# Optimization experiments

Hardware: AMD Instinct MI355X
Metric: run time of the kernel (lower is better)

Reference implementation:

```python
import jax, jax.numpy as jnp
import numpy as np

B, S, D = 2, 2048, 1024
H, DK, DV = 16, 64, 64
DFF = 4096
EPS_RMS = 1e-6


def setup_inputs() -> dict:
    key = jax.random.key(0)
    ks = jax.random.split(key, 10)
    sc = 0.02
    return {
        "x": jax.random.normal(ks[0], (B, S, D), jnp.float32),
        "w_q": jax.random.normal(ks[1], (D, H * DK), jnp.float32) * sc,
        "w_k": jax.random.normal(ks[2], (D, H * DK), jnp.float32) * sc,
        "w_v": jax.random.normal(ks[3], (D, H * DV), jnp.float32) * sc,
        "w_o": jax.random.normal(ks[4], (H * DV, D), jnp.float32) * sc,
        "w_gate": jax.random.normal(ks[5], (D, DFF), jnp.float32) * sc,
        "w_up": jax.random.normal(ks[6], (D, DFF), jnp.float32) * sc,
        "w_down": jax.random.normal(ks[7], (DFF, D), jnp.float32) * sc,
        "g1": jnp.ones((D,), jnp.float32),
        "g2": jnp.ones((D,), jnp.float32),
    }


def _rmsnorm(x, g):
    var = jnp.mean(jnp.square(x), axis=-1, keepdims=True)
    return x * jax.lax.rsqrt(var + EPS_RMS) * g


def _stable_softmax(s):
    # Faithful to source: exp(x) / (sum exp(x) + 1e-9); fully-masked rows -> 0.
    e = jnp.exp(s)
    return e / (jnp.sum(e, axis=-1, keepdims=True) + 1e-9)


def reference(x, w_q, w_k, w_v, w_o, w_gate, w_up, w_down, g1, g2):
    b, s, d = x.shape
    h = _rmsnorm(x, g1)
    q = (h @ w_q).reshape(b, s, H, DK).transpose(0, 2, 1, 3)  # [B,H,S,DK]
    k = (h @ w_k).reshape(b, s, H, DK).transpose(0, 2, 1, 3)
    v = (h @ w_v).reshape(b, s, H, DV).transpose(0, 2, 1, 3)
    scores = jnp.einsum("bhqd,bhkd->bhqk", q, k) / jnp.sqrt(jnp.asarray(DK, x.dtype))
    # triu with diagonal=0: self and future positions are masked
    mask = jnp.triu(jnp.ones((s, s), bool))
    scores = jnp.where(mask, -jnp.inf, scores)
    attn = _stable_softmax(scores)  # [B,H,S,S]
    av = jnp.einsum("bhqk,bhkd->bhqd", attn, v)
    av = av.transpose(0, 2, 1, 3).reshape(b, s, H * DV)
    x = x + av @ w_o  # residual 1
    h2 = _rmsnorm(x, g2)
    hidden = jax.nn.silu(h2 @ w_gate) * (h2 @ w_up)
    return x + hidden @ w_down  # residual 2
```

## Files before the change

### kernel.cpp

```cpp
#include <hip/hip_runtime.h>
#include <cstdint>
#include <cstddef>

typedef unsigned short u16;
typedef unsigned char u8;
typedef unsigned int u32;
typedef __bf16 bf16x8 __attribute__((ext_vector_type(8)));
typedef float floatx4 __attribute__((ext_vector_type(4)));
typedef float floatx16 __attribute__((ext_vector_type(16)));
typedef int i32x8 __attribute__((ext_vector_type(8)));

#define B_ 2
#define S_ 2048
#define D_ 1024
#define H_ 16
#define DFF_ 4096
#define BS_ 4096

__device__ __forceinline__ u16 f2bf(float f) {
  u32 u = __builtin_bit_cast(u32, f);
  u += 0x7fffu + ((u >> 16) & 1u);
  return (u16)(u >> 16);
}
__device__ __forceinline__ float bf2f(u16 h) {
  u32 u = ((u32)h) << 16;
  return __builtin_bit_cast(float, u);
}

__device__ __forceinline__ u32 cvtpk_bf16(float lo, float hi) {
  u32 r;
  asm("v_cvt_pk_bf16_f32 %0, %1, %2" : "=v"(r) : "v"(lo), "v"(hi));
  return r;
}

__device__ __forceinline__ float fexp2(float x) {
  float r;
  asm("v_exp_f32 %0, %1" : "=v"(r) : "v"(x));
  return r;
}

__device__ __forceinline__ u32 f2e4m3(float f) {
  u32 u = __builtin_bit_cast(u32, f);
  const u32 s = (u >> 24) & 0x80u;
  const u32 au = u & 0x7fffffffu;
  if (au < 0x3c800000u) return s;
  if (au > 0x43e00000u) return s | 0x7eu;
  const u32 lsb = (au >> 20) & 1u;
  const u32 r = au + 0x0007ffffu + lsb;
  const u32 e = (r >> 23) & 0xffu;
  const u32 m = (r >> 20) & 7u;
  return s | (((e - 120u) & 0xfu) << 3) | m;
}

__device__ __forceinline__ void gl_lds16(const void* g, void* l) {
  __builtin_amdgcn_global_load_lds(
      (const __attribute__((address_space(1))) void*)g,
      (__attribute__((address_space(3))) void*)l, 16, 0, 0);
}

__device__ __forceinline__ void xcd_swz(int GX, int GY, int& bx, int& by) {
  int flat = by * GX + bx;
  const int q = (GX * GY) >> 3;
  flat = (flat & 7) * q + (flat >> 3);
  bx = flat % GX;
  by = flat / GX;
}

#define WAITB(N) asm volatile("s_waitcnt vmcnt(" #N ")\n\ts_barrier" ::: "memory")

__global__ void prep_weights(const float* __restrict__ wq, const float* __restrict__ wk,
                             const float* __restrict__ wv, const float* __restrict__ wo,
                             const float* __restrict__ wg, const float* __restrict__ wu,
                             const float* __restrict__ wd,
                             u16* __restrict__ wqkv_t, u16* __restrict__ wo_t,
                             u8* __restrict__ wguf8, u16* __restrict__ wdn_t) {
  __shared__ float tile[32][33];
  const int id = blockIdx.x;
  const float* src;
  u16* dst = nullptr;
  int R, C, bx, by, mode;
  if (id < 3072) {
    const int which = id >> 10, lo = id & 1023;
    src = which == 0 ? wq : (which == 1 ? wk : wv);
    dst = wqkv_t + which * 1024 * 1024;
    R = 1024; C = 1024; bx = lo & 31; by = lo >> 5; mode = 0;
  } else if (id < 4096) {
    const int lo = id - 3072;
    src = wo; dst = wo_t; R = 1024; C = 1024; bx = lo & 31; by = lo >> 5; mode = 0;
  } else if (id < 8192) {
    const int lo = id - 4096;
    src = wg; R = 1024; C = 4096; bx = lo & 127; by = lo >> 7; mode = 1;
  } else if (id < 12288) {
    const int lo = id - 8192;
    src = wu; R = 1024; C = 4096; bx = lo & 127; by = lo >> 7; mode = 2;
  } else {
    const int lo = id - 12288;
    src = wd; dst = wdn_t; R = 4096; C = 1024; bx = lo & 31; by = lo >> 5; mode = 0;
  }
  const int tx = threadIdx.x, ty = threadIdx.y;
  const int c0 = bx * 32, r0 = by * 32;
#pragma unroll
  for (int i = 0; i < 4; i++)
    tile[ty + i * 8][tx] = src[(size_t)(r0 + ty + i * 8) * C + c0 + tx];
  __syncthreads();
  const int sx = ty * 32 + tx;
  const int oci = sx >> 3, cg = (sx & 7) * 4;
  const int oc = c0 + oci;
  const float v0 = tile[cg][oci], v1 = tile[cg + 1][oci];
  const float v2 = tile[cg + 2][oci], v3 = tile[cg + 3][oci];
  if (mode == 0) {
    uint2 o;
    o.x = (u32)f2bf(v0) | ((u32)f2bf(v1) << 16);
    o.y = (u32)f2bf(v2) | ((u32)f2bf(v3) << 16);
    *(uint2*)(dst + (size_t)oc * R + r0 + cg) = o;
  } else {
    const int orow = (oc >> 5) * 64 + (oc & 31) + (mode == 2 ? 32 : 0);
    const u32 p = f2e4m3(v0 * 64.f) | (f2e4m3(v1 * 64.f) << 8) |
                  (f2e4m3(v2 * 64.f) << 16) | (f2e4m3(v3 * 64.f) << 24);
    *(u32*)(wguf8 + (size_t)orow * 1024 + r0 + cg) = p;
  }
}

template <int F8>
__global__ __launch_bounds__(256) void rmsnorm_kernel(const float* __restrict__ x,
                                                      const float* __restrict__ g,
                                                      void* __restrict__ out) {
  const int row = blockIdx.x, t = threadIdx.x;
  const float4 v = ((const float4*)(x + (size_t)row * 1024))[t];
  float ss = v.x * v.x + v.y * v.y + v.z * v.z + v.w * v.w;
#pragma unroll
  for (int off = 32; off > 0; off >>= 1) ss += __shfl_xor(ss, off);
  __shared__ float red[4];
  if ((t & 63) == 0) red[t >> 6] = ss;
  __syncthreads();
  ss = red[0] + red[1] + red[2] + red[3];
  const float inv = rsqrtf(ss * (1.0f / 1024.0f) + 1e-6f);
  const float4 gv = ((const float4*)g)[t];
  const float y0 = v.x * inv * gv.x, y1 = v.y * inv * gv.y;
  const float y2 = v.z * inv * gv.z, y3 = v.w * inv * gv.w;
  if (F8) {
    const u32 p = f2e4m3(y0) | (f2e4m3(y1) << 8) | (f2e4m3(y2) << 16) | (f2e4m3(y3) << 24);
    const int k = t * 4;
    const u32 ofs = (u32)(((row >> 5) * 16 + (k >> 6)) * 2048 +
                          ((k >> 5) & 1) * 1024 + (row & 31) * 32 + (k & 31));
    *(u32*)((u8*)out + ofs) = p;
  } else {
    uint2 o;
    o.x = (u32)f2bf(y0) | ((u32)f2bf(y1) << 16);
    o.y = (u32)f2bf(y2) | ((u32)f2bf(y3) << 16);
    ((uint2*)out)[(size_t)row * 256 + t] = o;
  }
}

template <int BN>
__device__ __forceinline__ void bt_step(const u16* Asb, const u16* Bsb,
                                        floatx16 (&acc)[2][BN / 64],
                                        int wm, int wn, int c31, int khalf) {
  constexpr int NTI = BN / 64;
#pragma unroll
  for (int ks = 0; ks < 4; ks++) {
    bf16x8 af[2], bfr[NTI];
#pragma unroll
    for (int mi = 0; mi < 2; mi++) {
      const int row = wm * 64 + mi * 32 + c31;
      const int e = (ks * 2 + khalf) ^ (row & 7);
      af[mi] = *(const bf16x8*)(Asb + row * 64 + e * 8);
    }
#pragma unroll
    for (int ni = 0; ni < NTI; ni++) {
      const int row = wn * (BN / 2) + ni * 32 + c31;
      const int e = (ks * 2 + khalf) ^ (row & 7);
      bfr[ni] = *(const bf16x8*)(Bsb + row * 64 + e * 8);
    }
#pragma unroll
    for (int mi = 0; mi < 2; mi++)
#pragma unroll
      for (int ni = 0; ni < NTI; ni++)
        acc[mi][ni] = __builtin_amdgcn_mfma_f32_32x32x16_bf16(af[mi], bfr[ni],
                                                              acc[mi][ni], 0, 0, 0);
  }
}

template <int SPW>
__device__ __forceinline__ void bt_issue(const u16* (&gsrc)[SPW], u16* const (&ld0)[SPW],
                                         int bufofs) {
#pragma unroll
  for (int i = 0; i < SPW; i++) gl_lds16(gsrc[i], ld0[i] + bufofs);
#pragma unroll
  for (int i = 0; i < SPW; i++) gsrc[i] += 64;
}

template <int BN, int EPI>
__global__ __launch_bounds__(256) void gemm_bt(const u16* __restrict__ A,
                                               const u16* __restrict__ Bt,
                                               void* __restrict__ Cout,
                                               const float* __restrict__ res,
                                               u16* __restrict__ vTout,
                                               int M, int N, int K) {
  constexpr int NTI = BN / 64;
  constexpr int ASZ = 128 * 64;
  constexpr int STRIDE = ASZ + BN * 64;
  constexpr int NBUF = (BN == 64) ? 3 : 2;
  __shared__ u16 SMEM[NBUF * STRIDE];
  constexpr int NSEG = 16 + BN / 8;
  constexpr int SPW = NSEG / 4;
  const int t = threadIdx.x, w = t >> 6, l = t & 63;

  int bx = (int)blockIdx.x, by = (int)blockIdx.y;
  xcd_swz((int)gridDim.x, (int)gridDim.y, bx, by);
  const int m0 = by * 128, n0 = bx * BN;
  const int wm = w >> 1, wn = w & 1;
  const int c31 = l & 31, khalf = l >> 5;

  const u16* gsrc[SPW];
  u16* ld0[SPW];
  {
    const int rl = l >> 3, ch = (l & 7) ^ rl;
#pragma unroll
    for (int i = 0; i < SPW; i++) {
      const int s = w * SPW + i;
      if (s < 16) {
        gsrc[i] = A + (size_t)(m0 + s * 8 + rl) * K + ch * 8;
        ld0[i] = SMEM + s * 512;
      } else {
        gsrc[i] = Bt + (size_t)(n0 + (s - 16) * 8 + rl) * K + ch * 8;
        ld0[i] = SMEM + ASZ + (s - 16) * 512;
      }
    }
  }

  floatx16 acc[2][NTI] = {};

#define BT_STEP(CB) bt_step<BN>(SMEM + (CB)*STRIDE, SMEM + (CB)*STRIDE + ASZ, \
                                acc, wm, wn, c31, khalf)

  if constexpr (BN == 64) {
    bt_issue<SPW>(gsrc, ld0, 0 * STRIDE);
    bt_issue<SPW>(gsrc, ld0, 1 * STRIDE);
    const int NT = K >> 6;
    for (int rep = 0; rep < (NT - 4) / 3; rep++) {
      WAITB(6); bt_issue<SPW>(gsrc, ld0, 2 * STRIDE); BT_STEP(0);
      WAITB(6); bt_issue<SPW>(gsrc, ld0, 0 * STRIDE); BT_STEP(1);
      WAITB(6); bt_issue<SPW>(gsrc, ld0, 1 * STRIDE); BT_STEP(2);
    }
    WAITB(6); bt_issue<SPW>(gsrc, ld0, 2 * STRIDE); BT_STEP(0);
    WAITB(6); bt_issue<SPW>(gsrc, ld0, 0 * STRIDE); BT_STEP(1);
    WAITB(6); BT_STEP(2);
    WAITB(0); BT_STEP(0);
  } else {
    bt_issue<SPW>(gsrc, ld0, 0 * STRIDE);
    bt_issue<SPW>(gsrc, ld0, 1 * STRIDE);
    const int NT = K >> 6;
    for (int kk = 0; kk < NT - 2; kk += 2) {
      WAITB(8); BT_STEP(0);
      __builtin_amdgcn_s_barrier();
      bt_issue<SPW>(gsrc, ld0, 0 * STRIDE);
      WAITB(8); BT_STEP(1);
      __builtin_amdgcn_s_barrier();
      bt_issue<SPW>(gsrc, ld0, 1 * STRIDE);
    }
    WAITB(8); BT_STEP(0);
    WAITB(0); BT_STEP(1);
  }
#undef BT_STEP

  if constexpr (EPI == 3) {
    if (n0 >= 2048) {
#pragma unroll
      for (int mi = 0; mi < 2; mi++)
#pragma unroll
        for (int ni = 0; ni < NTI; ni++) {
          const int col = n0 + wn * (BN / 2) + ni * 32 + c31 - 2048;
          const int hh = col >> 6, dv = col & 63;
          const int rbase = m0 + wm * 64 + mi * 32 + 4 * khalf;
          const int bb = rbase >> 11;
          u16* vp = vTout + (size_t)((bb * 16 + hh) * 64 + dv) * 2048 + (rbase & 2047);
#pragma unroll
          for (int rg = 0; rg < 4; rg++) {
            uint2 pk;
            pk.x = (u32)f2bf(acc[mi][ni][rg * 4 + 0]) |
                   ((u32)f2bf(acc[mi][ni][rg * 4 + 1]) << 16);
            pk.y = (u32)f2bf(acc[mi][ni][rg * 4 + 2]) |
                   ((u32)f2bf(acc[mi][ni][rg * 4 + 3]) << 16);
            *(uint2*)(vp + rg * 8) = pk;
          }
        }
      return;
    }
  }
#pragma unroll
  for (int mi = 0; mi < 2; mi++)
#pragma unroll
    for (int ni = 0; ni < NTI; ni++) {
      const int col = n0 + wn * (BN / 2) + ni * 32 + c31;
#pragma unroll
      for (int reg = 0; reg < 16; reg++) {
        const int row = m0 + wm * 64 + mi * 32 + (reg & 3) + 8 * (reg >> 2) + 4 * khalf;
        const size_t idx = (size_t)row * N + col;
        if (EPI == 1) ((float*)Cout)[idx] = acc[mi][ni][reg] + res[idx];
        else          ((u16*)Cout)[idx] = f2bf(acc[mi][ni][reg]);
      }
    }
}

__global__ __launch_bounds__(256) void gemm_f8(const u8* __restrict__ Af,
                                               const u8* __restrict__ Bg,
                                               u16* __restrict__ hid,
                                               int M, int K) {
  constexpr int BSZ = 8192;
  __shared__ u8 SMEM[3 * BSZ];
  const int t = threadIdx.x, w = t >> 6, l = t & 63;
  int bx, by;
  {
    const int flat = (int)blockIdx.y * 64 + (int)blockIdx.x;
    const int xcd = flat & 7, seq = flat >> 3;
    const int bxl = seq & 15, byl = (seq >> 4) & 3, bxg = seq >> 6;
    bx = bxg * 16 + bxl;
    by = xcd * 4 + byl;
  }
  const int m0 = by * 128, n0 = bx * 128;
  const int wm = w >> 1, wn = w & 1;
  const int c31 = l & 31, hf = l >> 5;

  const u8* gsrcB[2];
  u32 ldofsB[2];
  {
    const int rl = l >> 2, ch = (l & 3) ^ ((l >> 3) & 3);
#pragma unroll
    for (int i = 0; i < 2; i++) {
      const int s = w * 2 + i;
      gsrcB[i] = Bg + (size_t)(n0 + s * 16 + rl) * K + ch * 16;
      ldofsB[i] = (u32)(s * 1024);
    }
  }
  const u8* Acur[2];
#pragma unroll
  for (int mi = 0; mi < 2; mi++)
    Acur[mi] = Af + (size_t)((by * 4 + wm * 2 + mi) * 16) * 2048 + l * 32;

  floatx16 acc[2][2] = {};
  i32x8 afr[3][2];

#define F8_LDA(SL)                                                      \
  do {                                                                  \
    _Pragma("unroll") for (int mi = 0; mi < 2; mi++) {                  \
      const uint4 lo = *(const uint4*)(Acur[mi]);                       \
      const uint4 hi = *(const uint4*)(Acur[mi] + 16);                  \
      afr[SL][mi] = i32x8{(int)lo.x, (int)lo.y, (int)lo.z, (int)lo.w,   \
                          (int)hi.x, (int)hi.y, (int)hi.z, (int)hi.w};  \
      Acur[mi] += 2048;                                                 \
    }                                                                   \
  } while (0)

#define F8_STB(SL)                                              \
  do {                                                          \
    _Pragma("unroll") for (int i = 0; i < 2; i++) {             \
      gl_lds16(gsrcB[i], SMEM + (SL)*BSZ + ldofsB[i]);          \
      gsrcB[i] += 64;                                           \
    }                                                           \
  } while (0)

#define F8_CMP(SL)                                                             \
  do {                                                                         \
    const u8* Bs = SMEM + (SL)*BSZ;                                            \
    i32x8 bfv[2];                                                              \
    _Pragma("unroll") for (int ni = 0; ni < 2; ni++) {                         \
      const int r = wn * 64 + ni * 32 + c31;                                   \
      const int g = (r >> 1) & 3;                                              \
      const uint4 lo = *(const uint4*)(Bs + r * 64 + ((2 * hf) ^ g) * 16);     \
      const uint4 hi = *(const uint4*)(Bs + r * 64 + ((2 * hf + 1) ^ g) * 16); \
      bfv[ni] = i32x8{(int)lo.x, (int)lo.y, (int)lo.z, (int)lo.w,              \
                      (int)hi.x, (int)hi.y, (int)hi.z, (int)hi.w};             \
    }                                                                          \
    _Pragma("unroll") for (int mi = 0; mi < 2; mi++)                           \
      _Pragma("unroll") for (int ni = 0; ni < 2; ni++)                         \
        acc[mi][ni] = __builtin_amdgcn_mfma_scale_f32_32x32x64_f8f6f4(         \
            afr[SL][mi], bfv[ni], acc[mi][ni], 0, 0,                           \
            0, 0x7F7F7F7F,                                    \
            0, 0x79797979);         \
  } while (0)

  F8_LDA(0); F8_STB(0);
  F8_LDA(1); F8_STB(1);
  for (int rep = 0; rep < 4; rep++) {
    WAITB(6); F8_LDA(2); F8_STB(2); F8_CMP(0);
    WAITB(6); F8_LDA(0); F8_STB(0); F8_CMP(1);
    WAITB(6); F8_LDA(1); F8_STB(1); F8_CMP(2);
  }
  WAITB(6); F8_LDA(2); F8_STB(2); F8_CMP(0);
  WAITB(6); F8_LDA(0); F8_STB(0); F8_CMP(1);
  WAITB(6); F8_CMP(2);
  WAITB(0); F8_CMP(0);
#undef F8_LDA
#undef F8_STB
#undef F8_CMP

#pragma unroll
  for (int mi = 0; mi < 2; mi++) {
    const int colo = (bx * 2 + wn) * 32 + c31;
#pragma unroll
    for (int reg = 0; reg < 16; reg++) {
      const int row = m0 + wm * 64 + mi * 32 + (reg & 3) + 8 * (reg >> 2) + 4 * hf;
      const float g = acc[mi][0][reg];
      const float u = acc[mi][1][reg];
      hid[(size_t)row * 4096 + colo] = f2bf(g / (1.f + __expf(-g)) * u);
    }
  }
}

__global__ __launch_bounds__(256) void attn_kernel(const u16* __restrict__ qkv,
                                                   const u16* __restrict__ vT,
                                                   u16* __restrict__ av) {
  __shared__ u16 SM[2 * 8192];
  __shared__ u16 Ps[4 * 2048];
  const int t = threadIdx.x, w = t >> 6, l = t & 63;
  const int lrow = l & 15, lk = l >> 4;
  const int bh = blockIdx.x;
  const int b = bh >> 4, h = bh & 15;
  u16* Pw = Ps + w * 2048;
  const float SC = 0.125f * 1.44269504088896f;

  for (int pass = 0; pass < 2; pass++) {
    const int qt = pass == 0 ? (15 - (int)blockIdx.y) : (int)blockIdx.y;
    const int qbase = qt * 128 + w * 32;
    const int ktmax = 2 * qt + 1;

    __syncthreads();

    bf16x8 aq[2][2];
#pragma unroll
    for (int sub = 0; sub < 2; sub++)
#pragma unroll
      for (int half = 0; half < 2; half++)
        aq[sub][half] = *(const bf16x8*)(qkv + (size_t)(b * S_ + qbase + sub * 16 + lrow) * 3072 +
                                         h * 64 + half * 32 + lk * 8);

    const u16* gcur[4];
    int gstep[4], loff[4];
#pragma unroll
    for (int i = 0; i < 4; i++) {
      const int c = w + 4 * i;
      const int half = (c >> 2) & 1, grp = c & 3;
      if (c < 8) {
        gcur[i] = qkv + (size_t)(b * S_ + grp * 16 + (l >> 2)) * 3072 + D_ + h * 64 +
                  half * 32 + (l & 3) * 8;
        gstep[i] = 64 * 3072;
        loff[i] = half * 2048 + grp * 512;
      } else {
        gcur[i] = vT + (size_t)(bh * 64 + grp * 16 + (l >> 2)) * S_ + half * 32 + (l & 3) * 8;
        gstep[i] = 64;
        loff[i] = 4096 + half * 2048 + grp * 512;
      }
    }

    floatx4 oacc[2][4] = {};
    float den[2] = {0.f, 0.f};

    int cur = 0;
#pragma unroll
    for (int i = 0; i < 4; i++) { gl_lds16(gcur[i], SM + loff[i]); gcur[i] += gstep[i]; }

    for (int kt = 0; kt <= ktmax; kt++) {
      __syncthreads();
      if (kt < ktmax) {
#pragma unroll
        for (int i = 0; i < 4; i++) {
          gl_lds16(gcur[i], SM + (cur ^ 1) * 8192 + loff[i]);
          gcur[i] += gstep[i];
        }
      }
      const u16* Kbuf = SM + cur * 8192;
      const u16* Vbuf = Kbuf + 4096;

      const bool active = (kt * 64 < qbase + 31);
      if (active) {
        const bool need_mask = (kt * 64 + 64 > qbase);

        bf16x8 bk[4][2];
#pragma unroll
        for (int ct = 0; ct < 4; ct++)
#pragma unroll
          for (int half = 0; half < 2; half++)
            bk[ct][half] = *(const bf16x8*)(Kbuf + half * 2048 + (ct * 16 + lrow) * 32 + lk * 8);

        floatx4 sf[2][4] = {};
        __builtin_amdgcn_s_setprio(1);
#pragma unroll
        for (int sub = 0; sub < 2; sub++)
#pragma unroll
          for (int ct = 0; ct < 4; ct++) {
            sf[sub][ct] = __builtin_amdgcn_mfma_f32_16x16x32_bf16(bk[ct][0], aq[sub][0],
                                                                  sf[sub][ct], 0, 0, 0);
            sf[sub][ct] = __builtin_amdgcn_mfma_f32_16x16x32_bf16(bk[ct][1], aq[sub][1],
                                                                  sf[sub][ct], 0, 0, 0);
          }
        __builtin_amdgcn_s_setprio(0);

        if (!need_mask) {
#pragma unroll
          for (int sub = 0; sub < 2; sub++) {
            const int prow = sub * 16 + lrow;
#pragma unroll
            for (int ct = 0; ct < 4; ct++) {
              const float p0 = fexp2(sf[sub][ct][0] * SC);
              const float p1 = fexp2(sf[sub][ct][1] * SC);
              const float p2 = fexp2(sf[sub][ct][2] * SC);
              const float p3 = fexp2(sf[sub][ct][3] * SC);
              den[sub] += (p0 + p1) + (p2 + p3);
              uint2 pk;
              pk.x = cvtpk_bf16(p0, p1);
              pk.y = cvtpk_bf16(p2, p3);
              *(uint2*)(Pw + prow * 64 + (((2 * ct + (lk >> 1)) ^ (lrow & 7)) << 3) +
                        (lk & 1) * 4) = pk;
            }
          }
        } else {
#pragma unroll
          for (int sub = 0; sub < 2; sub++) {
            const int qp = qbase + sub * 16 + lrow;
            const int prow = sub * 16 + lrow;
#pragma unroll
            for (int ct = 0; ct < 4; ct++) {
              const int kb = kt * 64 + ct * 16 + lk * 4;
              const float p0 = (kb + 0 < qp) ? fexp2(sf[sub][ct][0] * SC) : 0.f;
              const float p1 = (kb + 1 < qp) ? fexp2(sf[sub][ct][1] * SC) : 0.f;
              const float p2 = (kb + 2 < qp) ? fexp2(sf[sub][ct][2] * SC) : 0.f;
              const float p3 = (kb + 3 < qp) ? fexp2(sf[sub][ct][3] * SC) : 0.f;
              den[sub] += (p0 + p1) + (p2 + p3);
              uint2 pk;
              pk.x = cvtpk_bf16(p0, p1);
              pk.y = cvtpk_bf16(p2, p3);
              *(uint2*)(Pw + prow * 64 + (((2 * ct + (lk >> 1)) ^ (lrow & 7)) << 3) +
                        (lk & 1) * 4) = pk;
            }
          }
        }

        bf16x8 ap[2][2], bv[4][2];
#pragma unroll
        for (int sub = 0; sub < 2; sub++)
#pragma unroll
          for (int kh = 0; kh < 2; kh++) {
            const int prow = sub * 16 + lrow;
            ap[sub][kh] = *(const bf16x8*)(Pw + prow * 64 + (((kh * 4 + lk) ^ (prow & 7)) << 3));
          }
#pragma unroll
        for (int ni = 0; ni < 4; ni++)
#pragma unroll
          for (int kh = 0; kh < 2; kh++)
            bv[ni][kh] = *(const bf16x8*)(Vbuf + kh * 2048 + (ni * 16 + lrow) * 32 + lk * 8);
        __builtin_amdgcn_s_setprio(1);
#pragma unroll
        for (int sub = 0; sub < 2; sub++)
#pragma unroll
          for (int ni = 0; ni < 4; ni++) {
            oacc[sub][ni] = __builtin_amdgcn_mfma_f32_16x16x32_bf16(ap[sub][0], bv[ni][0],
                                                                    oacc[sub][ni], 0, 0, 0);
            oacc[sub][ni] = __builtin_amdgcn_mfma_f32_16x16x32_bf16(ap[sub][1], bv[ni][1],
                                                                    oacc[sub][ni], 0, 0, 0);
          }
        __builtin_amdgcn_s_setprio(0);
      }
      cur ^= 1;
    }

#pragma unroll
    for (int sub = 0; sub < 2; sub++) {
      den[sub] += __shfl_xor(den[sub], 16);
      den[sub] += __shfl_xor(den[sub], 32);
    }
    float dq[2][4];
#pragma unroll
    for (int sub = 0; sub < 2; sub++)
#pragma unroll
      for (int r = 0; r < 4; r++)
        dq[sub][r] = __shfl(den[sub], lk * 4 + r);

#pragma unroll
    for (int sub = 0; sub < 2; sub++)
#pragma unroll
      for (int ni = 0; ni < 4; ni++)
#pragma unroll
        for (int r = 0; r < 4; r++) {
          const int row = qbase + sub * 16 + lk * 4 + r;
          const int col = h * 64 + ni * 16 + lrow;
          av[(size_t)(b * S_ + row) * 1024 + col] = f2bf(oacc[sub][ni][r] / (dq[sub][r] + 1e-9f));
        }
  }
}

#define OFF_WQKV 0u
#define OFF_WO   6291456u
#define OFF_WGU8 8388608u
#define OFF_WDN  16777216u
#define OFF_H1   25165824u
#define OFF_QKV  33554432u
#define OFF_VT   58720256u
#define OFF_AV   67108864u
#define OFF_X1   75497472u
#define OFF_H2F8 92274688u
#define OFF_HID  96468992u

extern "C" void kernel_launch(void* const* d_in, const int* in_sizes, int n_in,
                              void* d_out, int out_size, void* d_ws, size_t ws_size,
                              hipStream_t stream) {
  const float* x      = (const float*)d_in[0];
  const float* w_q    = (const float*)d_in[1];
  const float* w_k    = (const float*)d_in[2];
  const float* w_v    = (const float*)d_in[3];
  const float* w_o    = (const float*)d_in[4];
  const float* w_gate = (const float*)d_in[5];
  const float* w_up   = (const float*)d_in[6];
  const float* w_down = (const float*)d_in[7];
  const float* g1     = (const float*)d_in[8];
  const float* g2     = (const float*)d_in[9];

  char* ws = (char*)d_ws;
  u16* wqkv_t = (u16*)(ws + OFF_WQKV);
  u16* wo_t   = (u16*)(ws + OFF_WO);
  u8*  wguf8  = (u8*)(ws + OFF_WGU8);
  u16* wdn_t  = (u16*)(ws + OFF_WDN);
  u16* h1     = (u16*)(ws + OFF_H1);
  u16* qkv    = (u16*)(ws + OFF_QKV);
  u16* vT     = (u16*)(ws + OFF_VT);
  u16* av     = (u16*)(ws + OFF_AV);
  float* x1   = (float*)(ws + OFF_X1);
  u8*  h2f8   = (u8*)(ws + OFF_H2F8);
  u16* hid    = (u16*)(ws + OFF_HID);
  float* out  = (float*)d_out;

  prep_weights<<<16384, dim3(32, 8), 0, stream>>>(w_q, w_k, w_v, w_o, w_gate, w_up, w_down,
                                                  wqkv_t, wo_t, wguf8, wdn_t);

  rmsnorm_kernel<0><<<BS_, 256, 0, stream>>>(x, g1, h1);
  gemm_bt<128, 3><<<dim3(3072 / 128, BS_ / 128), 256, 0, stream>>>(
      h1, wqkv_t, qkv, nullptr, vT, BS_, 3072, 1024);
  attn_kernel<<<dim3(32, 8), 256, 0, stream>>>(qkv, vT, av);
  gemm_bt<64, 1><<<dim3(1024 / 64, BS_ / 128), 256, 0, stream>>>(
      av, wo_t, x1, x, nullptr, BS_, 1024, 1024);
  rmsnorm_kernel<1><<<BS_, 256, 0, stream>>>(x1, g2, h2f8);
  gemm_f8<<<dim3(64, 32), 256, 0, stream>>>(h2f8, wguf8, hid, BS_, 1024);
  gemm_bt<64, 1><<<dim3(1024 / 64, BS_ / 128), 256, 0, stream>>>(
      hid, wdn_t, out, x1, nullptr, BS_, 1024, 4096);
}
```

Baseline: 337.3 us.

## Restructure attention to single-wave blocks loading K/V directly from global

Attention blocks change from 4-wave blocks, which share K/V tiles through double-buffered LDS with barriers and process two paired query tiles, to single-wave blocks each owning 32 query rows. K and V are now read straight from global memory into registers, with K prefetched one tile ahead using ping-pong register sets. This removes block-level synchronisation and gives 2048 small blocks for finer load balance under the causal mask. In exchange, cross-wave reuse of K/V in LDS is lost, so global/L2 traffic rises, and the explicit balanced pairing of short and long query tiles is gone.

```diff
diff --git a/kernel.cpp b/kernel.cpp
--- a/kernel.cpp
+++ b/kernel.cpp
@@ -408,185 +408,148 @@
   }
 }
 
-__global__ __launch_bounds__(256) void attn_kernel(const u16* __restrict__ qkv,
-                                                   const u16* __restrict__ vT,
-                                                   u16* __restrict__ av) {
-  __shared__ u16 SM[2 * 8192];
-  __shared__ u16 Ps[4 * 2048];
-  const int t = threadIdx.x, w = t >> 6, l = t & 63;
+__device__ __forceinline__ void attn_ldK(bf16x8 (&dst)[4][2], const u16* kbase, int kt) {
+#pragma unroll
+  for (int ct = 0; ct < 4; ct++)
+#pragma unroll
+    for (int hf = 0; hf < 2; hf++)
+      dst[ct][hf] = *(const bf16x8*)(kbase + (size_t)(kt * 64 + ct * 16) * 3072 + hf * 32);
+}
+__device__ __forceinline__ void attn_ldV(bf16x8 (&dst)[4][2], const u16* vbase, int kt) {
+#pragma unroll
+  for (int ni = 0; ni < 4; ni++)
+#pragma unroll
+    for (int kh = 0; kh < 2; kh++)
+      dst[ni][kh] = *(const bf16x8*)(vbase + (size_t)(ni * 16) * 2048 + kt * 64 + kh * 32);
+}
+
+__global__ __launch_bounds__(64, 2) void attn_kernel(const u16* __restrict__ qkv,
+                                                     const u16* __restrict__ vT,
+                                                     u16* __restrict__ av) {
+  __shared__ u16 Pw[2048];
+  const int l = threadIdx.x;
   const int lrow = l & 15, lk = l >> 4;
   const int bh = blockIdx.x;
+  const int j = blockIdx.y;
   const int b = bh >> 4, h = bh & 15;
-  u16* Pw = Ps + w * 2048;
+  const int qbase = j * 32;
+  const int NT = (qbase + 30) / 64 + 1;
   const float SC = 0.125f * 1.44269504088896f;
 
-  for (int pass = 0; pass < 2; pass++) {
-    const int qt = pass == 0 ? (15 - (int)blockIdx.y) : (int)blockIdx.y;
-    const int qbase = qt * 128 + w * 32;
-    const int ktmax = 2 * qt + 1;
-
-    __syncthreads();
-
-    bf16x8 aq[2][2];
-#pragma unroll
-    for (int sub = 0; sub < 2; sub++)
-#pragma unroll
-      for (int half = 0; half < 2; half++)
-        aq[sub][half] = *(const bf16x8*)(qkv + (size_t)(b * S_ + qbase + sub * 16 + lrow) * 3072 +
-                                         h * 64 + half * 32 + lk * 8);
-
-    const u16* gcur[4];
-    int gstep[4], loff[4];
-#pragma unroll
-    for (int i = 0; i < 4; i++) {
-      const int c = w + 4 * i;
-      const int half = (c >> 2) & 1, grp = c & 3;
-      if (c < 8) {
-        gcur[i] = qkv + (size_t)(b * S_ + grp * 16 + (l >> 2)) * 3072 + D_ + h * 64 +
-                  half * 32 + (l & 3) * 8;
-        gstep[i] = 64 * 3072;
-        loff[i] = half * 2048 + grp * 512;
-      } else {
-        gcur[i] = vT + (size_t)(bh * 64 + grp * 16 + (l >> 2)) * S_ + half * 32 + (l & 3) * 8;
-        gstep[i] = 64;
-        loff[i] = 4096 + half * 2048 + grp * 512;
+  bf16x8 aq[2][2];
+#pragma unroll
+  for (int sub = 0; sub < 2; sub++)
+#pragma unroll
+    for (int half = 0; half < 2; half++)
+      aq[sub][half] = *(const bf16x8*)(qkv + (size_t)(b * S_ + qbase + sub * 16 + lrow) * 3072 +
+                                       h * 64 + half * 32 + lk * 8);
+
+  const u16* kbase = qkv + (size_t)(b * S_ + lrow) * 3072 + D_ + h * 64 + lk * 8;
+  const u16* vbase = vT + (size_t)(bh * 64 + lrow) * 2048 + lk * 8;
+
+  floatx4 oacc[2][4] = {};
+  float den[2] = {0.f, 0.f};
+
+#define ATTN_BODY(KC, KN, KT, DOLOADN)                                         \
+  do {                                                                         \
+    bf16x8 bv[4][2];                                                           \
+    attn_ldV(bv, vbase, (KT));                                                 \
+    if (DOLOADN) attn_ldK(KN, kbase, (KT) + 1);                                \
+    floatx4 sf[2][4] = {};                                                     \
+    __builtin_amdgcn_s_setprio(1);                                             \
+    _Pragma("unroll") for (int sub = 0; sub < 2; sub++)                        \
+      _Pragma("unroll") for (int ct = 0; ct < 4; ct++) {                       \
+        sf[sub][ct] = __builtin_amdgcn_mfma_f32_16x16x32_bf16(                 \
+            KC[ct][0], aq[sub][0], sf[sub][ct], 0, 0, 0);                      \
+        sf[sub][ct] = __builtin_amdgcn_mfma_f32_16x16x32_bf16(                 \
+            KC[ct][1], aq[sub][1], sf[sub][ct], 0, 0, 0);                      \
+      }                                                                        \
+    __builtin_amdgcn_s_setprio(0);                                             \
+    if ((KT)*64 + 64 <= qbase) {                                               \
+      _Pragma("unroll") for (int sub = 0; sub < 2; sub++) {                    \
+        const int prow = sub * 16 + lrow;                                      \
+        _Pragma("unroll") for (int ct = 0; ct < 4; ct++) {                     \
+          const float p0 = fexp2(sf[sub][ct][0] * SC);                         \
+          const float p1 = fexp2(sf[sub][ct][1] * SC);                         \
+          const float p2 = fexp2(sf[sub][ct][2] * SC);                         \
+          const float p3 = fexp2(sf[sub][ct][3] * SC);                         \
+          den[sub] += (p0 + p1) + (p2 + p3);                                   \
+          uint2 pk;                                                            \
+          pk.x = cvtpk_bf16(p0, p1);                                           \
+          pk.y = cvtpk_bf16(p2, p3);                                           \
+          *(uint2*)(Pw + prow * 64 + (((2 * ct + (lk >> 1)) ^ (lrow & 7)) << 3) + \
+                    (lk & 1) * 4) = pk;                                        \
+        }                                                                      \
+      }                                                                        \
+    } else {                                                                   \
+      _Pragma("unroll") for (int sub = 0; sub < 2; sub++) {                    \
+        const int qp = qbase + sub * 16 + lrow;                                \
+        const int prow = sub * 16 + lrow;                                      \
+        _Pragma("unroll") for (int ct = 0; ct < 4; ct++) {                     \
+          const int kb = (KT) * 64 + ct * 16 + lk * 4;                         \
+          const float p0 = (kb + 0 < qp) ? fexp2(sf[sub][ct][0] * SC) : 0.f;   \
+          const float p1 = (kb + 1 < qp) ? fexp2(sf[sub][ct][1] * SC) : 0.f;   \
+          const float p2 = (kb + 2 < qp) ? fexp2(sf[sub][ct][2] * SC) : 0.f;   \
+          const float p3 = (kb + 3 < qp) ? fexp2(sf[sub][ct][3] * SC) : 0.f;   \
+          den[sub] += (p0 + p1) + (p2 + p3);                                   \
+          uint2 pk;                                                            \
+          pk.x = cvtpk_bf16(p0, p1);                                           \
+          pk.y = cvtpk_bf16(p2, p3);                                           \
+          *(uint2*)(Pw + prow * 64 + (((2 * ct + (lk >> 1)) ^ (lrow & 7)) << 3) + \
+                    (lk & 1) * 4) = pk;                                        \
+        }                                                                      \
+      }                                                                        \
+    }                                                                          \
+    bf16x8 ap[2][2];                                                           \
+    _Pragma("unroll") for (int sub = 0; sub < 2; sub++)                        \
+      _Pragma("unroll") for (int kh = 0; kh < 2; kh++) {                       \
+        const int prow = sub * 16 + lrow;                                      \
+        ap[sub][kh] = *(const bf16x8*)(Pw + prow * 64 +                        \
+                                       (((kh * 4 + lk) ^ (prow & 7)) << 3));   \
+      }                                                                        \
+    __builtin_amdgcn_s_setprio(1);                                             \
+    _Pragma("unroll") for (int sub = 0; sub < 2; sub++)                        \
+      _Pragma("unroll") for (int ni = 0; ni < 4; ni++) {                       \
+        oacc[sub][ni] = __builtin_amdgcn_mfma_f32_16x16x32_bf16(               \
+            ap[sub][0], bv[ni][0], oacc[sub][ni], 0, 0, 0);                    \
+        oacc[sub][ni] = __builtin_amdgcn_mfma_f32_16x16x32_bf16(               \
+            ap[sub][1], bv[ni][1], oacc[sub][ni], 0, 0, 0);                    \
+      }                                                                        \
+    __builtin_amdgcn_s_setprio(0);                                             \
+  } while (0)
+
+  bf16x8 bkA[4][2], bkB[4][2];
+  attn_ldK(bkA, kbase, 0);
+  int kt = 0;
+  for (; kt + 2 <= NT; kt += 2) {
+    ATTN_BODY(bkA, bkB, kt, true);
+    ATTN_BODY(bkB, bkA, kt + 1, (kt + 3 <= NT));
+  }
+  if (kt < NT) ATTN_BODY(bkA, bkB, kt, false);
+#undef ATTN_BODY
+
+#pragma unroll
+  for (int sub = 0; sub < 2; sub++) {
+    den[sub] += __shfl_xor(den[sub], 16);
+    den[sub] += __shfl_xor(den[sub], 32);
+  }
+  float dq[2][4];
+#pragma unroll
+  for (int sub = 0; sub < 2; sub++)
+#pragma unroll
+    for (int r = 0; r < 4; r++)
+      dq[sub][r] = __shfl(den[sub], lk * 4 + r);
+
+#pragma unroll
+  for (int sub = 0; sub < 2; sub++)
+#pragma unroll
+    for (int ni = 0; ni < 4; ni++)
+#pragma unroll
+      for (int r = 0; r < 4; r++) {
+        const int row = qbase + sub * 16 + lk * 4 + r;
+        const int col = h * 64 + ni * 16 + lrow;
+        av[(size_t)(b * S_ + row) * 1024 + col] = f2bf(oacc[sub][ni][r] / (dq[sub][r] + 1e-9f));
       }
-    }
-
-    floatx4 oacc[2][4] = {};
-    float den[2] = {0.f, 0.f};
-
-    int cur = 0;
-#pragma unroll
-    for (int i = 0; i < 4; i++) { gl_lds16(gcur[i], SM + loff[i]); gcur[i] += gstep[i]; }
-
-    for (int kt = 0; kt <= ktmax; kt++) {
-      __syncthreads();
-      if (kt < ktmax) {
-#pragma unroll
-        for (int i = 0; i < 4; i++) {
-          gl_lds16(gcur[i], SM + (cur ^ 1) * 8192 + loff[i]);
-          gcur[i] += gstep[i];
-        }
-      }
-      const u16* Kbuf = SM + cur * 8192;
-      const u16* Vbuf = Kbuf + 4096;
-
-      const bool active = (kt * 64 < qbase + 31);
-      if (active) {
-        const bool need_mask = (kt * 64 + 64 > qbase);
-
-        bf16x8 bk[4][2];
-#pragma unroll
-        for (int ct = 0; ct < 4; ct++)
-#pragma unroll
-          for (int half = 0; half < 2; half++)
-            bk[ct][half] = *(const bf16x8*)(Kbuf + half * 2048 + (ct * 16 + lrow) * 32 + lk * 8);
-
-        floatx4 sf[2][4] = {};
-        __builtin_amdgcn_s_setprio(1);
-#pragma unroll
-        for (int sub = 0; sub < 2; sub++)
-#pragma unroll
-          for (int ct = 0; ct < 4; ct++) {
-            sf[sub][ct] = __builtin_amdgcn_mfma_f32_16x16x32_bf16(bk[ct][0], aq[sub][0],
-                                                                  sf[sub][ct], 0, 0, 0);
-            sf[sub][ct] = __builtin_amdgcn_mfma_f32_16x16x32_bf16(bk[ct][1], aq[sub][1],
-                                                                  sf[sub][ct], 0, 0, 0);
-          }
-        __builtin_amdgcn_s_setprio(0);
-
-        if (!need_mask) {
-#pragma unroll
-          for (int sub = 0; sub < 2; sub++) {
-            const int prow = sub * 16 + lrow;
-#pragma unroll
-            for (int ct = 0; ct < 4; ct++) {
-              const float p0 = fexp2(sf[sub][ct][0] * SC);
-              const float p1 = fexp2(sf[sub][ct][1] * SC);
-              const float p2 = fexp2(sf[sub][ct][2] * SC);
-              const float p3 = fexp2(sf[sub][ct][3] * SC);
-              den[sub] += (p0 + p1) + (p2 + p3);
-              uint2 pk;
-              pk.x = cvtpk_bf16(p0, p1);
-              pk.y = cvtpk_bf16(p2, p3);
-              *(uint2*)(Pw + prow * 64 + (((2 * ct + (lk >> 1)) ^ (lrow & 7)) << 3) +
-                        (lk & 1) * 4) = pk;
-            }
-          }
-        } else {
-#pragma unroll
-          for (int sub = 0; sub < 2; sub++) {
-            const int qp = qbase + sub * 16 + lrow;
-            const int prow = sub * 16 + lrow;
-#pragma unroll
-            for (int ct = 0; ct < 4; ct++) {
-              const int kb = kt * 64 + ct * 16 + lk * 4;
-              const float p0 = (kb + 0 < qp) ? fexp2(sf[sub][ct][0] * SC) : 0.f;
-              const float p1 = (kb + 1 < qp) ? fexp2(sf[sub][ct][1] * SC) : 0.f;
-              const float p2 = (kb + 2 < qp) ? fexp2(sf[sub][ct][2] * SC) : 0.f;
-              const float p3 = (kb + 3 < qp) ? fexp2(sf[sub][ct][3] * SC) : 0.f;
-              den[sub] += (p0 + p1) + (p2 + p3);
-              uint2 pk;
-              pk.x = cvtpk_bf16(p0, p1);
-              pk.y = cvtpk_bf16(p2, p3);
-              *(uint2*)(Pw + prow * 64 + (((2 * ct + (lk >> 1)) ^ (lrow & 7)) << 3) +
-                        (lk & 1) * 4) = pk;
-            }
-          }
-        }
-
-        bf16x8 ap[2][2], bv[4][2];
-#pragma unroll
-        for (int sub = 0; sub < 2; sub++)
-#pragma unroll
-          for (int kh = 0; kh < 2; kh++) {
-            const int prow = sub * 16 + lrow;
-            ap[sub][kh] = *(const bf16x8*)(Pw + prow * 64 + (((kh * 4 + lk) ^ (prow & 7)) << 3));
-          }
-#pragma unroll
-        for (int ni = 0; ni < 4; ni++)
-#pragma unroll
-          for (int kh = 0; kh < 2; kh++)
-            bv[ni][kh] = *(const bf16x8*)(Vbuf + kh * 2048 + (ni * 16 + lrow) * 32 + lk * 8);
-        __builtin_amdgcn_s_setprio(1);
-#pragma unroll
-        for (int sub = 0; sub < 2; sub++)
-#pragma unroll
-          for (int ni = 0; ni < 4; ni++) {
-            oacc[sub][ni] = __builtin_amdgcn_mfma_f32_16x16x32_bf16(ap[sub][0], bv[ni][0],
-                                                                    oacc[sub][ni], 0, 0, 0);
-            oacc[sub][ni] = __builtin_amdgcn_mfma_f32_16x16x32_bf16(ap[sub][1], bv[ni][1],
-                                                                    oacc[sub][ni], 0, 0, 0);
-          }
-        __builtin_amdgcn_s_setprio(0);
-      }
-      cur ^= 1;
-    }
-
-#pragma unroll
-    for (int sub = 0; sub < 2; sub++) {
-      den[sub] += __shfl_xor(den[sub], 16);
-      den[sub] += __shfl_xor(den[sub], 32);
-    }
-    float dq[2][4];
-#pragma unroll
-    for (int sub = 0; sub < 2; sub++)
-#pragma unroll
-      for (int r = 0; r < 4; r++)
-        dq[sub][r] = __shfl(den[sub], lk * 4 + r);
-
-#pragma unroll
-    for (int sub = 0; sub < 2; sub++)
-#pragma unroll
-      for (int ni = 0; ni < 4; ni++)
-#pragma unroll
-        for (int r = 0; r < 4; r++) {
-          const int row = qbase + sub * 16 + lk * 4 + r;
-          const int col = h * 64 + ni * 16 + lrow;
-          av[(size_t)(b * S_ + row) * 1024 + col] = f2bf(oacc[sub][ni][r] / (dq[sub][r] + 1e-9f));
-        }
-  }
 }
 
 #define OFF_WQKV 0u
@@ -635,7 +598,7 @@
   rmsnorm_kernel<0><<<BS_, 256, 0, stream>>>(x, g1, h1);
   gemm_bt<128, 3><<<dim3(3072 / 128, BS_ / 128), 256, 0, stream>>>(
       h1, wqkv_t, qkv, nullptr, vT, BS_, 3072, 1024);
-  attn_kernel<<<dim3(32, 8), 256, 0, stream>>>(qkv, vT, av);
+  attn_kernel<<<dim3(32, 64), 64, 0, stream>>>(qkv, vT, av);
   gemm_bt<64, 1><<<dim3(1024 / 64, BS_ / 128), 256, 0, stream>>>(
       av, wo_t, x1, x, nullptr, BS_, 1024, 1024);
   rmsnorm_kernel<1><<<BS_, 256, 0, stream>>>(x1, g2, h2f8);
```

After: 349.9 us. 1.04x slower.

## Write SwiGLU hidden in MFMA fragment layout and load A directly to registers

Applied to the files above, without the earlier changes.

The gate/up FP8 GEMM epilogue now stores the bf16 hidden activations in a pre-swizzled fragment-major layout that matches the 32x32x16 MFMA A-operand. A new down-projection GEMM variant reads A straight from global memory into registers, with triple-buffered register sets, and stages only B through LDS. This removes LDS traffic and sync for the A tile in the K=4096 down projection. In exchange it uses more registers and makes the producer and consumer kernels depend on a shared layout.

```diff
diff --git a/kernel.cpp b/kernel.cpp
--- a/kernel.cpp
+++ b/kernel.cpp
@@ -303,6 +303,97 @@
     }
 }
 
+template <int EPI>
+__global__ __launch_bounds__(256) void gemm_btA(const u16* __restrict__ Afm,
+                                                const u16* __restrict__ Bt,
+                                                void* __restrict__ Cout,
+                                                const float* __restrict__ res,
+                                                int M, int N, int K) {
+  constexpr int BSZ = 64 * 64;
+  __shared__ u16 SMEM[3 * BSZ];
+  const int t = threadIdx.x, w = t >> 6, l = t & 63;
+  int bx = (int)blockIdx.x, by = (int)blockIdx.y;
+  xcd_swz((int)gridDim.x, (int)gridDim.y, bx, by);
+  const int m0 = by * 128, n0 = bx * 64;
+  const int wm = w >> 1, wn = w & 1;
+  const int c31 = l & 31, khalf = l >> 5;
+  const int brow = wn * 32 + c31;
+
+  const u16* gsrcB[2];
+  u32 ldofsB[2];
+  {
+    const int rl = l >> 3, ch = (l & 7) ^ rl;
+#pragma unroll
+    for (int i = 0; i < 2; i++) {
+      const int s = w * 2 + i;
+      gsrcB[i] = Bt + (size_t)(n0 + s * 8 + rl) * K + ch * 8;
+      ldofsB[i] = (u32)(s * 512);
+    }
+  }
+  const u16* Abase[2];
+#pragma unroll
+  for (int mi = 0; mi < 2; mi++)
+    Abase[mi] = Afm + (size_t)((m0 >> 5) + wm * 2 + mi) * (size_t)(K >> 4) * 512 + l * 8;
+
+  floatx16 acc[2] = {};
+  bf16x8 areg0[2][4], areg1[2][4], areg2[2][4];
+
+#define A_LD(AR, T)                                                      \
+  do {                                                                   \
+    _Pragma("unroll") for (int mi = 0; mi < 2; mi++)                     \
+      _Pragma("unroll") for (int ks = 0; ks < 4; ks++)                   \
+        AR[mi][ks] = *(const bf16x8*)(Abase[mi] + ((T) * 4 + ks) * 512); \
+  } while (0)
+
+#define B_ST(SL)                                                \
+  do {                                                          \
+    _Pragma("unroll") for (int i = 0; i < 2; i++) {             \
+      gl_lds16(gsrcB[i], SMEM + (SL)*BSZ + ldofsB[i]);          \
+      gsrcB[i] += 64;                                           \
+    }                                                           \
+  } while (0)
+
+#define CMPT(AR, SL)                                                           \
+  do {                                                                         \
+    _Pragma("unroll") for (int ks = 0; ks < 4; ks++) {                         \
+      const int e = (ks * 2 + khalf) ^ (brow & 7);                             \
+      const bf16x8 bfr = *(const bf16x8*)(SMEM + (SL)*BSZ + brow * 64 + e * 8);\
+      _Pragma("unroll") for (int mi = 0; mi < 2; mi++)                         \
+        acc[mi] = __builtin_amdgcn_mfma_f32_32x32x16_bf16(AR[mi][ks], bfr,     \
+                                                          acc[mi], 0, 0, 0);   \
+    }                                                                          \
+  } while (0)
+
+  A_LD(areg0, 0); B_ST(0);
+  A_LD(areg1, 1); B_ST(1);
+  const int NT = K >> 6;
+  int tt = 0;
+  for (int rep = 0; rep < (NT - 4) / 3; rep++) {
+    WAITB(10); A_LD(areg2, tt + 2); B_ST(2); CMPT(areg0, 0);
+    WAITB(10); A_LD(areg0, tt + 3); B_ST(0); CMPT(areg1, 1);
+    WAITB(10); A_LD(areg1, tt + 4); B_ST(1); CMPT(areg2, 2);
+    tt += 3;
+  }
+  WAITB(10); A_LD(areg2, tt + 2); B_ST(2); CMPT(areg0, 0);
+  WAITB(10); A_LD(areg0, tt + 3); B_ST(0); CMPT(areg1, 1);
+  WAITB(10); CMPT(areg2, 2);
+  WAITB(0);  CMPT(areg0, 0);
+#undef A_LD
+#undef B_ST
+#undef CMPT
+
+  const int col = n0 + wn * 32 + c31;
+#pragma unroll
+  for (int mi = 0; mi < 2; mi++)
+#pragma unroll
+    for (int reg = 0; reg < 16; reg++) {
+      const int row = m0 + wm * 64 + mi * 32 + (reg & 3) + 8 * (reg >> 2) + 4 * khalf;
+      const size_t idx = (size_t)row * N + col;
+      if (EPI == 1) ((float*)Cout)[idx] = acc[mi][reg] + res[idx];
+      else          ((u16*)Cout)[idx] = f2bf(acc[mi][reg]);
+    }
+}
+
 __global__ __launch_bounds__(256) void gemm_f8(const u8* __restrict__ Af,
                                                const u8* __restrict__ Bg,
                                                u16* __restrict__ hid,
@@ -395,15 +486,20 @@
 #undef F8_STB
 #undef F8_CMP
 
+  const int g0 = (m0 >> 5) + wm * 2;
+  const int colo = (bx * 2 + wn) * 32 + c31;
+  const int fcol = colo >> 4;
+  const int lhalf = (colo >> 3) & 1;
+  const int elem = colo & 7;
 #pragma unroll
   for (int mi = 0; mi < 2; mi++) {
-    const int colo = (bx * 2 + wn) * 32 + c31;
 #pragma unroll
     for (int reg = 0; reg < 16; reg++) {
-      const int row = m0 + wm * 64 + mi * 32 + (reg & 3) + 8 * (reg >> 2) + 4 * hf;
+      const int r31 = (reg & 3) + 8 * (reg >> 2) + 4 * hf;
       const float g = acc[mi][0][reg];
       const float u = acc[mi][1][reg];
-      hid[(size_t)row * 4096 + colo] = f2bf(g / (1.f + __expf(-g)) * u);
+      hid[((size_t)(g0 + mi) * 256 + fcol) * 512 + (r31 + 32 * lhalf) * 8 + elem] =
+          f2bf(g / (1.f + __expf(-g)) * u);
     }
   }
 }
@@ -640,6 +736,6 @@
       av, wo_t, x1, x, nullptr, BS_, 1024, 1024);
   rmsnorm_kernel<1><<<BS_, 256, 0, stream>>>(x1, g2, h2f8);
   gemm_f8<<<dim3(64, 32), 256, 0, stream>>>(h2f8, wguf8, hid, BS_, 1024);
-  gemm_bt<64, 1><<<dim3(1024 / 64, BS_ / 128), 256, 0, stream>>>(
-      hid, wdn_t, out, x1, nullptr, BS_, 1024, 4096);
-}
+  gemm_btA<1><<<dim3(1024 / 64, BS_ / 128), 256, 0, stream>>>(
+      hid, wdn_t, out, x1, BS_, 1024, 4096);
+}
```

New measurement: 352.2 us. +4.4%, slower.
